# Optimization experiments

Hardware: AMD Instinct MI355X
Metric: run time of the kernel (lower is better)

## Reference

```python
import jax, jax.numpy as jnp
import numpy as np

KERNEL_SIZE = 3

def setup_inputs() -> dict:
    key = jax.random.key(0)
    k1, k2, k3, k4, k5 = jax.random.split(key, 5)
    B, L, D, K = 4, 4096, 1024, KERNEL_SIZE
    x = jax.random.normal(k1, (B, L, D), dtype=jnp.float32)
    # depthwise conv: torch weight shape (D, 1, K) -> store as (D, K)
    fan_dw = 1.0 / np.sqrt(1 * K)
    w_dw = jax.random.uniform(k2, (D, K), dtype=jnp.float32, minval=-fan_dw, maxval=fan_dw)
    b_dw = jax.random.uniform(k3, (D,), dtype=jnp.float32, minval=-fan_dw, maxval=fan_dw)
    # pointwise conv: torch weight shape (D, D, 1) -> store as (D_out, D_in)
    fan_pw = 1.0 / np.sqrt(D * 1)
    w_pw = jax.random.uniform(k4, (D, D), dtype=jnp.float32, minval=-fan_pw, maxval=fan_pw)
    b_pw = jax.random.uniform(k5, (D,), dtype=jnp.float32, minval=-fan_pw, maxval=fan_pw)
    return {"x": x, "w_dw": w_dw, "b_dw": b_dw, "w_pw": w_pw, "b_pw": b_pw}

def _causal_dw_pw(x, w_dw, b_dw, w_pw, b_pw):
    # x: (B, L, D); causal left-pad by K-1 along L
    K = w_dw.shape[1]
    L = x.shape[1]
    xp = jnp.pad(x, ((0, 0), (K - 1, 0), (0, 0)))  # (B, L+K-1, D)
    # depthwise: y[b,l,d] = sum_k xp[b,l+k,d] * w_dw[d,k]
    y = sum(xp[:, k:k + L, :] * w_dw[:, k] for k in range(K)) + b_dw
    # pointwise 1x1 conv: mix channels
    return jnp.einsum('bld,ed->ble', y, w_pw) + b_pw

def reference(x, w_dw, b_dw, w_pw, b_pw):
    return _causal_dw_pw(x, w_dw, b_dw, w_pw, b_pw)
```

## Files before the change

kernel.cpp:

```cpp
#include <hip/hip_runtime.h>
#include <hip/hip_bf16.h>
#include <stdint.h>

#define B_SZ   4
#define L_SEQ  4096
#define D_DIM  1024
#define M_TOT  (B_SZ * L_SEQ)

typedef __bf16 bf16;
typedef __attribute__((ext_vector_type(8))) __bf16 bf16x8;
typedef __attribute__((ext_vector_type(4))) float   f32x4;

#define GLOAD_LDS16(g, l)                                                     \
  __builtin_amdgcn_global_load_lds(                                           \
      (const __attribute__((address_space(1))) void*)(g),                     \
      (__attribute__((address_space(3))) void*)(l), 16, 0, 0)

__global__ __launch_bounds__(256) void dw_bf16_kernel(
    const float* __restrict__ x, const float* __restrict__ w_dw,
    const float* __restrict__ b_dw, bf16* __restrict__ y) {
  const int t  = threadIdx.x;
  const int b  = blockIdx.x >> 8;
  const int lc = blockIdx.x & 255;
  const int l0 = lc * 16;
  const int d0 = t * 4;

  float w0[4], w1[4], w2[4], bias[4];
#pragma unroll
  for (int c = 0; c < 4; ++c) {
    int d = d0 + c;
    w0[c] = w_dw[d * 3 + 0];
    w1[c] = w_dw[d * 3 + 1];
    w2[c] = w_dw[d * 3 + 2];
    bias[c] = b_dw[d];
  }

  const float* xb = x + (size_t)b * L_SEQ * D_DIM;
  bf16*        yb = y + (size_t)b * L_SEQ * D_DIM;

  float4 xm2 = make_float4(0.f, 0.f, 0.f, 0.f);
  float4 xm1 = make_float4(0.f, 0.f, 0.f, 0.f);
  if (l0 >= 2) xm2 = *(const float4*)(xb + (size_t)(l0 - 2) * D_DIM + d0);
  if (l0 >= 1) xm1 = *(const float4*)(xb + (size_t)(l0 - 1) * D_DIM + d0);

#pragma unroll 4
  for (int i = 0; i < 16; ++i) {
    int l = l0 + i;
    float4 xc = *(const float4*)(xb + (size_t)l * D_DIM + d0);
    float a0 = fmaf(xm2.x, w0[0], fmaf(xm1.x, w1[0], fmaf(xc.x, w2[0], bias[0])));
    float a1 = fmaf(xm2.y, w0[1], fmaf(xm1.y, w1[1], fmaf(xc.y, w2[1], bias[1])));
    float a2 = fmaf(xm2.z, w0[2], fmaf(xm1.z, w1[2], fmaf(xc.z, w2[2], bias[2])));
    float a3 = fmaf(xm2.w, w0[3], fmaf(xm1.w, w1[3], fmaf(xc.w, w2[3], bias[3])));
    union { bf16 h[4]; int2 v; } o;
    o.h[0] = (bf16)a0; o.h[1] = (bf16)a1; o.h[2] = (bf16)a2; o.h[3] = (bf16)a3;
    *(int2*)(yb + (size_t)l * D_DIM + d0) = o.v;
    xm2 = xm1;
    xm1 = xc;
  }
}

__global__ __launch_bounds__(256) void cvt_bf16_kernel(
    const float* __restrict__ w, bf16* __restrict__ o) {
  int i = (blockIdx.x * 256 + threadIdx.x) * 8;
  float4 a = *(const float4*)(w + i);
  float4 b = *(const float4*)(w + i + 4);
  union { bf16 h[8]; int4 v; } r;
  r.h[0] = (bf16)a.x; r.h[1] = (bf16)a.y; r.h[2] = (bf16)a.z; r.h[3] = (bf16)a.w;
  r.h[4] = (bf16)b.x; r.h[5] = (bf16)b.y; r.h[6] = (bf16)b.z; r.h[7] = (bf16)b.w;
  *(int4*)(o + i) = r.v;
}

#define BM 128
#define BN 128
#define BK 64
#define EP_ROWP 68

__global__ __launch_bounds__(256) void gemm_bt_kernel(
    const bf16* __restrict__ A,
    const bf16* __restrict__ Bm,
    const float* __restrict__ bias, float* __restrict__ C) {
  __shared__ __align__(16) char smem[32768];
  bf16* Asm = (bf16*)smem;
  bf16* Bsm = (bf16*)(smem + 16384);

  const int t    = threadIdx.x;
  const int m0   = blockIdx.x * BM;
  const int n0   = blockIdx.y * BN;
  const int lane = t & 63;
  const int wv   = t >> 6;
  const int wm   = (wv >> 1) * 64;
  const int wn   = (wv & 1) * 64;
  const int lrow = lane & 15;
  const int q    = lane >> 4;

  f32x4 acc[4][4] = {};

  int srow[4], sgc[4];
#pragma unroll
  for (int i = 0; i < 4; ++i) {
    int s   = i * 256 + t;
    srow[i] = s >> 3;
    sgc[i]  = (s & 7) ^ (srow[i] & 7);
  }

  for (int k0 = 0; k0 < D_DIM; k0 += BK) {
    __syncthreads();
#pragma unroll
    for (int i = 0; i < 4; ++i) {
      unsigned lds_off = (unsigned)(i * 4096 + wv * 1024);
      const bf16* ga = A  + (size_t)(m0 + srow[i]) * D_DIM + k0 + sgc[i] * 8;
      const bf16* gb = Bm + (size_t)(n0 + srow[i]) * D_DIM + k0 + sgc[i] * 8;
      GLOAD_LDS16(ga, (char*)Asm + lds_off);
      GLOAD_LDS16(gb, (char*)Bsm + lds_off);
    }
    __syncthreads();

#pragma unroll
    for (int kk = 0; kk < 2; ++kk) {
      bf16x8 af[4], bfr[4];
#pragma unroll
      for (int i = 0; i < 4; ++i) {
        int mrow = wm + i * 16 + lrow;
        int ck   = (kk * 4 + q) ^ (mrow & 7);
        af[i] = *(const bf16x8*)((const char*)Asm + (size_t)mrow * (BK * 2) + ck * 16);
        int nrow = wn + i * 16 + lrow;
        int ckb  = (kk * 4 + q) ^ (nrow & 7);
        bfr[i] = *(const bf16x8*)((const char*)Bsm + (size_t)nrow * (BK * 2) + ckb * 16);
      }
#pragma unroll
      for (int i = 0; i < 4; ++i)
#pragma unroll
        for (int j = 0; j < 4; ++j)
          acc[i][j] = __builtin_amdgcn_mfma_f32_16x16x32_bf16(af[i], bfr[j], acc[i][j], 0, 0, 0);
    }
  }

  __syncthreads();
  float* ep = (float*)smem + (size_t)wv * (16 * EP_ROWP);

  float bvj[4];
#pragma unroll
  for (int j = 0; j < 4; ++j) bvj[j] = bias[n0 + wn + j * 16 + lrow];

#pragma unroll
  for (int i = 0; i < 4; ++i) {
#pragma unroll
    for (int j = 0; j < 4; ++j)
#pragma unroll
      for (int r = 0; r < 4; ++r)
        ep[(q * 4 + r) * EP_ROWP + j * 16 + lrow] = acc[i][j][r] + bvj[j];
#pragma unroll
    for (int it = 0; it < 4; ++it) {
      int flat = it * 64 + lane;
      int row  = flat >> 4;
      int c4   = flat & 15;
      float4 v = *(const float4*)(ep + row * EP_ROWP + c4 * 4);
      int gm = m0 + wm + i * 16 + row;
      int gn = n0 + wn + c4 * 4;
      *(float4*)(C + (size_t)gm * D_DIM + gn) = v;
    }
    __syncthreads();
  }
}

__global__ __launch_bounds__(256) void fallback_kernel(
    const float* __restrict__ x, const float* __restrict__ w_dw,
    const float* __restrict__ b_dw, const float* __restrict__ w_pw,
    const float* __restrict__ b_pw, float* __restrict__ out) {
  __shared__ float ys[D_DIM];
  const int m = blockIdx.x;
  const int l = m & (L_SEQ - 1);
  const int t = threadIdx.x;
  const float* xr = x + (size_t)m * D_DIM;
#pragma unroll
  for (int c = 0; c < 4; ++c) {
    int d = t + c * 256;
    float a = fmaf(xr[d], w_dw[d * 3 + 2], b_dw[d]);
    if (l >= 1) a = fmaf(xr[d - D_DIM], w_dw[d * 3 + 1], a);
    if (l >= 2) a = fmaf(xr[d - 2 * D_DIM], w_dw[d * 3 + 0], a);
    ys[d] = a;
  }
  __syncthreads();
#pragma unroll
  for (int c = 0; c < 4; ++c) {
    int e = t + c * 256;
    const float* wr = w_pw + (size_t)e * D_DIM;
    float a = b_pw[e];
    for (int d = 0; d < D_DIM; ++d) a = fmaf(ys[d], wr[d], a);
    out[(size_t)m * D_DIM + e] = a;
  }
}

extern "C" void kernel_launch(void* const* d_in, const int* in_sizes, int n_in,
                              void* d_out, int out_size, void* d_ws, size_t ws_size,
                              hipStream_t stream) {
  (void)in_sizes; (void)n_in; (void)out_size;
  const float* x    = (const float*)d_in[0];
  const float* w_dw = (const float*)d_in[1];
  const float* b_dw = (const float*)d_in[2];
  const float* w_pw = (const float*)d_in[3];
  const float* b_pw = (const float*)d_in[4];
  float* out = (float*)d_out;

  const size_t y_elems = (size_t)M_TOT * D_DIM;
  const size_t w_elems = (size_t)D_DIM * D_DIM;
  const size_t need = (y_elems + w_elems) * sizeof(bf16);

  if (ws_size >= need) {
    bf16* y    = (bf16*)d_ws;
    bf16* wpwb = (bf16*)d_ws + y_elems;
    dw_bf16_kernel<<<B_SZ * (L_SEQ / 16), 256, 0, stream>>>(x, w_dw, b_dw, y);
    cvt_bf16_kernel<<<(D_DIM * D_DIM / 8) / 256, 256, 0, stream>>>(w_pw, wpwb);
    dim3 grid(M_TOT / BM, D_DIM / BN);
    gemm_bt_kernel<<<grid, 256, 0, stream>>>(y, wpwb, b_pw, out);
  } else {
    fallback_kernel<<<M_TOT, 256, 0, stream>>>(x, w_dw, b_dw, w_pw, b_pw, out);
  }
}
```

Baseline: 171.9 us.

## Double-buffer GEMM LDS tiles, fuse weight cast into depthwise kernel, swap grid order

The GEMM now uses BK=32 with two LDS buffers, so the next tile's global-to-LDS loads are issued while the current tile is computed, and there is one barrier per step instead of two. The grid is transposed so blocks sharing an M row panel run next to each other, which should improve L2 reuse of the activation tiles. The pointwise weight conversion is folded into the depthwise kernel as extra blocks, removing one launch. The depthwise kernel now handles one row per block and reloads neighbouring rows instead of streaming them, which trades more global reads for more parallelism.

Measured after the change: 204.6 us. 1.19x slower.

```diff
diff --git a/kernel.cpp b/kernel.cpp
--- a/kernel.cpp
+++ b/kernel.cpp
@@ -18,61 +18,48 @@
 
 __global__ __launch_bounds__(256) void dw_bf16_kernel(
     const float* __restrict__ x, const float* __restrict__ w_dw,
-    const float* __restrict__ b_dw, bf16* __restrict__ y) {
-  const int t  = threadIdx.x;
-  const int b  = blockIdx.x >> 8;
-  const int lc = blockIdx.x & 255;
-  const int l0 = lc * 16;
+    const float* __restrict__ b_dw, bf16* __restrict__ y,
+    const float* __restrict__ w_pw, bf16* __restrict__ wpwb) {
+  const int t = threadIdx.x;
+  if (blockIdx.x >= M_TOT) {
+    int i = ((blockIdx.x - M_TOT) * 256 + t) * 8;
+    float4 a = *(const float4*)(w_pw + i);
+    float4 b = *(const float4*)(w_pw + i + 4);
+    union { bf16 h[8]; int4 v; } r;
+    r.h[0] = (bf16)a.x; r.h[1] = (bf16)a.y; r.h[2] = (bf16)a.z; r.h[3] = (bf16)a.w;
+    r.h[4] = (bf16)b.x; r.h[5] = (bf16)b.y; r.h[6] = (bf16)b.z; r.h[7] = (bf16)b.w;
+    *(int4*)(wpwb + i) = r.v;
+    return;
+  }
+  const int m  = blockIdx.x;
+  const int l  = m & (L_SEQ - 1);
   const int d0 = t * 4;
-
-  float w0[4], w1[4], w2[4], bias[4];
-#pragma unroll
-  for (int c = 0; c < 4; ++c) {
-    int d = d0 + c;
-    w0[c] = w_dw[d * 3 + 0];
-    w1[c] = w_dw[d * 3 + 1];
-    w2[c] = w_dw[d * 3 + 2];
-    bias[c] = b_dw[d];
-  }
-
-  const float* xb = x + (size_t)b * L_SEQ * D_DIM;
-  bf16*        yb = y + (size_t)b * L_SEQ * D_DIM;
-
-  float4 xm2 = make_float4(0.f, 0.f, 0.f, 0.f);
-  float4 xm1 = make_float4(0.f, 0.f, 0.f, 0.f);
-  if (l0 >= 2) xm2 = *(const float4*)(xb + (size_t)(l0 - 2) * D_DIM + d0);
-  if (l0 >= 1) xm1 = *(const float4*)(xb + (size_t)(l0 - 1) * D_DIM + d0);
-
-#pragma unroll 4
-  for (int i = 0; i < 16; ++i) {
-    int l = l0 + i;
-    float4 xc = *(const float4*)(xb + (size_t)l * D_DIM + d0);
-    float a0 = fmaf(xm2.x, w0[0], fmaf(xm1.x, w1[0], fmaf(xc.x, w2[0], bias[0])));
-    float a1 = fmaf(xm2.y, w0[1], fmaf(xm1.y, w1[1], fmaf(xc.y, w2[1], bias[1])));
-    float a2 = fmaf(xm2.z, w0[2], fmaf(xm1.z, w1[2], fmaf(xc.z, w2[2], bias[2])));
-    float a3 = fmaf(xm2.w, w0[3], fmaf(xm1.w, w1[3], fmaf(xc.w, w2[3], bias[3])));
-    union { bf16 h[4]; int2 v; } o;
-    o.h[0] = (bf16)a0; o.h[1] = (bf16)a1; o.h[2] = (bf16)a2; o.h[3] = (bf16)a3;
-    *(int2*)(yb + (size_t)l * D_DIM + d0) = o.v;
-    xm2 = xm1;
-    xm1 = xc;
-  }
-}
-
-__global__ __launch_bounds__(256) void cvt_bf16_kernel(
-    const float* __restrict__ w, bf16* __restrict__ o) {
-  int i = (blockIdx.x * 256 + threadIdx.x) * 8;
-  float4 a = *(const float4*)(w + i);
-  float4 b = *(const float4*)(w + i + 4);
-  union { bf16 h[8]; int4 v; } r;
-  r.h[0] = (bf16)a.x; r.h[1] = (bf16)a.y; r.h[2] = (bf16)a.z; r.h[3] = (bf16)a.w;
-  r.h[4] = (bf16)b.x; r.h[5] = (bf16)b.y; r.h[6] = (bf16)b.z; r.h[7] = (bf16)b.w;
-  *(int4*)(o + i) = r.v;
+  const float* xr = x + (size_t)m * D_DIM + d0;
+
+  const float4 zero = make_float4(0.f, 0.f, 0.f, 0.f);
+  float4 x2 = (l >= 2) ? *(const float4*)(xr - 2 * D_DIM) : zero;
+  float4 x1 = (l >= 1) ? *(const float4*)(xr - D_DIM) : zero;
+  float4 x0 = *(const float4*)(xr);
+
+  const float* wp = w_dw + d0 * 3;
+  float4 wa = *(const float4*)(wp);
+  float4 wb = *(const float4*)(wp + 4);
+  float4 wc = *(const float4*)(wp + 8);
+  float4 bv = *(const float4*)(b_dw + d0);
+
+  float a0 = fmaf(x2.x, wa.x, fmaf(x1.x, wa.y, fmaf(x0.x, wa.z, bv.x)));
+  float a1 = fmaf(x2.y, wa.w, fmaf(x1.y, wb.x, fmaf(x0.y, wb.y, bv.y)));
+  float a2 = fmaf(x2.z, wb.z, fmaf(x1.z, wb.w, fmaf(x0.z, wc.x, bv.z)));
+  float a3 = fmaf(x2.w, wc.y, fmaf(x1.w, wc.z, fmaf(x0.w, wc.w, bv.w)));
+
+  union { bf16 h[4]; int2 v; } o;
+  o.h[0] = (bf16)a0; o.h[1] = (bf16)a1; o.h[2] = (bf16)a2; o.h[3] = (bf16)a3;
+  *(int2*)(y + (size_t)m * D_DIM + d0) = o.v;
 }
 
 #define BM 128
 #define BN 128
-#define BK 64
+#define BK 32
 #define EP_ROWP 68
 
 __global__ __launch_bounds__(256) void gemm_bt_kernel(
@@ -80,12 +67,10 @@
     const bf16* __restrict__ Bm,
     const float* __restrict__ bias, float* __restrict__ C) {
   __shared__ __align__(16) char smem[32768];
-  bf16* Asm = (bf16*)smem;
-  bf16* Bsm = (bf16*)(smem + 16384);
 
   const int t    = threadIdx.x;
-  const int m0   = blockIdx.x * BM;
-  const int n0   = blockIdx.y * BN;
+  const int n0   = blockIdx.x * BN;
+  const int m0   = blockIdx.y * BM;
   const int lane = t & 63;
   const int wv   = t >> 6;
   const int wm   = (wv >> 1) * 64;
@@ -95,44 +80,46 @@
 
   f32x4 acc[4][4] = {};
 
-  int srow[4], sgc[4];
-#pragma unroll
-  for (int i = 0; i < 4; ++i) {
+  int srow[2], sgc[2];
+#pragma unroll
+  for (int i = 0; i < 2; ++i) {
     int s   = i * 256 + t;
-    srow[i] = s >> 3;
-    sgc[i]  = (s & 7) ^ (srow[i] & 7);
-  }
-
-  for (int k0 = 0; k0 < D_DIM; k0 += BK) {
+    srow[i] = s >> 2;
+    sgc[i]  = (s & 3) ^ ((srow[i] >> 1) & 3);
+  }
+  const unsigned lbase = (unsigned)(wv * 1024);
+
+  auto stage = [&](int p, int k0) {
+#pragma unroll
+    for (int i = 0; i < 2; ++i) {
+      unsigned off = (unsigned)(p * 16384 + i * 4096) + lbase;
+      GLOAD_LDS16(A  + (size_t)(m0 + srow[i]) * D_DIM + k0 + sgc[i] * 8, smem + off);
+      GLOAD_LDS16(Bm + (size_t)(n0 + srow[i]) * D_DIM + k0 + sgc[i] * 8, smem + 8192 + off);
+    }
+  };
+
+  stage(0, 0);
+  for (int it = 0; it < D_DIM / BK; ++it) {
     __syncthreads();
+    if (it < D_DIM / BK - 1) stage((it + 1) & 1, (it + 1) * BK);
+    const char* Ab = smem + (it & 1) * 16384;
+    const char* Bb = Ab + 8192;
+
+    bf16x8 af[4], bfr[4];
 #pragma unroll
     for (int i = 0; i < 4; ++i) {
-      unsigned lds_off = (unsigned)(i * 4096 + wv * 1024);
-      const bf16* ga = A  + (size_t)(m0 + srow[i]) * D_DIM + k0 + sgc[i] * 8;
-      const bf16* gb = Bm + (size_t)(n0 + srow[i]) * D_DIM + k0 + sgc[i] * 8;
-      GLOAD_LDS16(ga, (char*)Asm + lds_off);
-      GLOAD_LDS16(gb, (char*)Bsm + lds_off);
+      int mrow = wm + i * 16 + lrow;
+      int ck   = q ^ ((mrow >> 1) & 3);
+      af[i] = *(const bf16x8*)(Ab + (size_t)mrow * (BK * 2) + ck * 16);
+      int nrow = wn + i * 16 + lrow;
+      int ckb  = q ^ ((nrow >> 1) & 3);
+      bfr[i] = *(const bf16x8*)(Bb + (size_t)nrow * (BK * 2) + ckb * 16);
     }
-    __syncthreads();
-
-#pragma unroll
-    for (int kk = 0; kk < 2; ++kk) {
-      bf16x8 af[4], bfr[4];
-#pragma unroll
-      for (int i = 0; i < 4; ++i) {
-        int mrow = wm + i * 16 + lrow;
-        int ck   = (kk * 4 + q) ^ (mrow & 7);
-        af[i] = *(const bf16x8*)((const char*)Asm + (size_t)mrow * (BK * 2) + ck * 16);
-        int nrow = wn + i * 16 + lrow;
-        int ckb  = (kk * 4 + q) ^ (nrow & 7);
-        bfr[i] = *(const bf16x8*)((const char*)Bsm + (size_t)nrow * (BK * 2) + ckb * 16);
-      }
-#pragma unroll
-      for (int i = 0; i < 4; ++i)
-#pragma unroll
-        for (int j = 0; j < 4; ++j)
-          acc[i][j] = __builtin_amdgcn_mfma_f32_16x16x32_bf16(af[i], bfr[j], acc[i][j], 0, 0, 0);
-    }
+#pragma unroll
+    for (int i = 0; i < 4; ++i)
+#pragma unroll
+      for (int j = 0; j < 4; ++j)
+        acc[i][j] = __builtin_amdgcn_mfma_f32_16x16x32_bf16(af[i], bfr[j], acc[i][j], 0, 0, 0);
   }
 
   __syncthreads();
@@ -209,9 +196,9 @@
   if (ws_size >= need) {
     bf16* y    = (bf16*)d_ws;
     bf16* wpwb = (bf16*)d_ws + y_elems;
-    dw_bf16_kernel<<<B_SZ * (L_SEQ / 16), 256, 0, stream>>>(x, w_dw, b_dw, y);
-    cvt_bf16_kernel<<<(D_DIM * D_DIM / 8) / 256, 256, 0, stream>>>(w_pw, wpwb);
-    dim3 grid(M_TOT / BM, D_DIM / BN);
+    const int cvt_blocks = (D_DIM * D_DIM / 8) / 256;
+    dw_bf16_kernel<<<M_TOT + cvt_blocks, 256, 0, stream>>>(x, w_dw, b_dw, y, w_pw, wpwb);
+    dim3 grid(D_DIM / BN, M_TOT / BM);
     gemm_bt_kernel<<<grid, 256, 0, stream>>>(y, wpwb, b_pw, out);
   } else {
     fallback_kernel<<<M_TOT, 256, 0, stream>>>(x, w_dw, b_dw, w_pw, b_pw, out);
```
